# Kernel optimization log

Measured on AMD Instinct MI355X. Metric: run time of the kernel, lower is better.

Reference implementation:

```python
import jax, jax.numpy as jnp
import numpy as np

V, B, T, H = 32000, 32, 128, 256  # vocab, batch, max seq len, RNN_HIDDEN_SIZE


def setup_inputs() -> dict:
    key = jax.random.key(0)
    ks = jax.random.split(key, 16)
    stdv = 1.0 / np.sqrt(H)
    u = lambda k, shape: jax.random.uniform(k, shape, jnp.float32, -stdv, stdv)
    return {
        "tokens": jax.random.randint(ks[0], (B, T), 0, V),          # argmax of one-hot packed data
        "lengths": jax.random.randint(ks[1], (B,), 1, T + 1),        # valid lengths per sequence
        "emb": jax.random.normal(ks[2], (V, H), jnp.float32),        # tied embedding / output proj
        "Wh0": u(ks[3], (H, H)), "Wx0": u(ks[4], (H, H)), "Wy0": u(ks[5], (H, H)),
        "bh0": jnp.zeros((H,), jnp.float32), "by0": jnp.zeros((H,), jnp.float32),
        "Wh1": u(ks[6], (H, H)), "Wx1": u(ks[7], (H, H)), "Wy1": u(ks[8], (H, H)),
        "bh1": jnp.zeros((H,), jnp.float32), "by1": jnp.zeros((H,), jnp.float32),
    }


def _rnn_cell(x, Wh, Wx, bh, Wy, by):
    # x: [B, T, H]. hidden = tanh(h @ Wh + x_t @ Wx + bh); Y_t = hidden @ Wy + by
    xw = jnp.einsum('bth,hk->btk', x, Wx) + bh  # precompute input projection for all steps
    h0 = jnp.zeros((x.shape[0], Wh.shape[1]), x.dtype)

    def step(h, xt):
        h = jnp.tanh(h @ Wh + xt)
        return h, h @ Wy + by

    _, ys = jax.lax.scan(step, h0, xw.transpose(1, 0, 2))  # [T, B, H]
    return ys.transpose(1, 0, 2)  # [B, T, H]


def reference(tokens, lengths, emb, Wh0, Wx0, Wy0, bh0, by0, Wh1, Wx1, Wy1, bh1, by1):
    x = emb[tokens]                                  # embedding lookup [B, T, H]
    h = _rnn_cell(x, Wh0, Wx0, bh0, Wy0, by0)        # RNNCell layer 0
    h = _rnn_cell(h, Wh1, Wx1, bh1, Wy1, by1)        # RNNCell layer 1
    logits = jnp.einsum('bth,vh->btv', h, emb)       # hidden.data @ embedding.weight.T
    probs = jax.nn.softmax(logits, axis=-1)          # softmax over vocab
    # emulate PackedSequence: zero out padded timesteps (packed data == masked positions)
    mask = (jnp.arange(T)[None, :] < lengths[:, None]).astype(probs.dtype)  # [B, T]
    return probs * mask[:, :, None], h * mask[:, :, None]
```

## Files before the change

kernel.cpp:

```cpp
#include <hip/hip_runtime.h>
#include <hip/hip_bf16.h>


typedef _Float16 f16x8 __attribute__((ext_vector_type(8)));
typedef _Float16 f16x4 __attribute__((ext_vector_type(4)));
typedef float f32x4 __attribute__((ext_vector_type(4)));

#define NROWS 4096
#define HDIM 256
#define VOC 32000
#define VT 128
#define NVT 250

__device__ __forceinline__ float tanh_fast(float x) {
    float e = __expf(2.f * x);
    return 1.f - 2.f / (e + 1.f);
}

__global__ __launch_bounds__(256) void cvt_kernel(const float* __restrict__ in,
                                                  _Float16* __restrict__ out, int n4) {
    int i = blockIdx.x * 256 + threadIdx.x;
    if (i < n4) {
        float4 v = ((const float4*)in)[i];
        f16x4 o = {(_Float16)v.x, (_Float16)v.y, (_Float16)v.z, (_Float16)v.w};
        ((f16x4*)out)[i] = o;
    }
}

__global__ __launch_bounds__(256) void wc_kernel(const float* __restrict__ Wy0,
                                                 const float* __restrict__ Wx1,
                                                 const float* __restrict__ by0,
                                                 const float* __restrict__ bh1,
                                                 float* __restrict__ Wc,
                                                 float* __restrict__ bc) {
    __shared__ float arow[HDIM];
    int i = blockIdx.x, n = threadIdx.x;
    const float* src = (i < HDIM) ? (Wy0 + i * HDIM) : by0;
    arow[n] = src[n];
    __syncthreads();
    float acc = 0.f;
#pragma unroll 8
    for (int j = 0; j < HDIM; ++j) acc += arow[j] * Wx1[j * HDIM + n];
    if (i < HDIM) Wc[i * HDIM + n] = acc;
    else bc[n] = acc + bh1[n];
}

__global__ __launch_bounds__(256) void gemm_rows(const float* __restrict__ A,
                                                 const int* __restrict__ tokens,
                                                 const float* __restrict__ emb,
                                                 const float* __restrict__ W,
                                                 const float* __restrict__ bias,
                                                 float* __restrict__ outp,
                                                 _Float16* __restrict__ y16,
                                                 const int* __restrict__ lengths) {
    __shared__ float As[16][HDIM];
    int tid = threadIdx.x;
    int r0 = blockIdx.x * 16;
#pragma unroll
    for (int i = 0; i < 16; ++i) {
        int row = r0 + i;
        float v;
        if (tokens) v = emb[(size_t)tokens[row] * HDIM + tid];
        else        v = A[(size_t)row * HDIM + tid];
        As[i][tid] = v;
    }
    __syncthreads();
    int n = tid;
    float acc[16];
#pragma unroll
    for (int r = 0; r < 16; ++r) acc[r] = 0.f;
#pragma unroll 4
    for (int j = 0; j < HDIM; ++j) {
        float wv = W[j * HDIM + n];
#pragma unroll
        for (int r = 0; r < 16; ++r) acc[r] += As[r][j] * wv;
    }
    float bb = bias[n];
#pragma unroll
    for (int r = 0; r < 16; ++r) {
        int row = r0 + r;
        float val = acc[r] + bb;
        if (y16) {
            y16[(size_t)row * HDIM + n] = (_Float16)val;
            int b = row >> 7, t = row & 127;
            outp[(size_t)row * HDIM + n] = (t < lengths[b]) ? val : 0.f;
        } else {
            outp[(size_t)row * HDIM + n] = val;
        }
    }
}

__global__ __launch_bounds__(1024, 4) void scan_kernel(const float* __restrict__ xw,
                                                       const float* __restrict__ Wh,
                                                       float* __restrict__ hseq) {
    int b = blockIdx.x;
    int tid = threadIdx.x;
    int k = tid & 255, q = tid >> 8;
    float w[64];
#pragma unroll
    for (int j = 0; j < 64; ++j) w[j] = Wh[(q * 64 + j) * HDIM + k];
    __shared__ float hbuf[2][HDIM];
    __shared__ float psum[4][HDIM];
    if (tid < HDIM) hbuf[0][tid] = 0.f;
    __syncthreads();
    const float* xwb = xw + (size_t)b * 128 * HDIM;
    float* hb = hseq + (size_t)b * 128 * HDIM;
    for (int t = 0; t < 128; ++t) {
        int cur = t & 1;
        float xwv = 0.f;
        if (tid < HDIM) xwv = xwb[t * HDIM + tid];
        const float4* h4 = (const float4*)(&hbuf[cur][q * 64]);
        float acc = 0.f;
#pragma unroll
        for (int jj = 0; jj < 16; ++jj) {
            float4 hv = h4[jj];
            acc += w[jj * 4 + 0] * hv.x + w[jj * 4 + 1] * hv.y +
                   w[jj * 4 + 2] * hv.z + w[jj * 4 + 3] * hv.w;
        }
        psum[q][k] = acc;
        __syncthreads();
        if (tid < HDIM) {
            float s = psum[0][tid] + psum[1][tid] + psum[2][tid] + psum[3][tid] + xwv;
            float hn = tanh_fast(s);
            hbuf[1 - cur][tid] = hn;
            hb[t * HDIM + tid] = hn;
        }
        __syncthreads();
    }
}

__global__ __launch_bounds__(256) void logits_kernel(const _Float16* __restrict__ y16,
                                                     const _Float16* __restrict__ emb16,
                                                     const int* __restrict__ lengths,
                                                     float* __restrict__ probs,
                                                     float* __restrict__ partials) {
    int rt = blockIdx.x, vt = blockIdx.y;
    int r0 = rt * 16, v0 = vt * VT;
    int b = r0 >> 7, t0 = r0 & 127;
    int len = lengths[b];
    int tid = threadIdx.x, lane = tid & 63, wv = tid >> 6;

    if (len <= t0) {
        float4 z = {0.f, 0.f, 0.f, 0.f};
#pragma unroll
        for (int i = 0; i < 2; ++i) {
            int fid = tid + i * 256;
            int rl = fid >> 5, c4 = fid & 31;
            ((float4*)(probs + (size_t)(r0 + rl) * VOC + v0))[c4] = z;
        }
        return;
    }

    f32x4 acc0 = {0.f, 0.f, 0.f, 0.f}, acc1 = {0.f, 0.f, 0.f, 0.f};
    int l15 = lane & 15, quad = lane >> 4;
    int kq = quad * 8;
    const f16x8* Ap = (const f16x8*)(y16 + (size_t)(r0 + l15) * HDIM + kq);
    int n0 = v0 + wv * 32;
    const f16x8* B0 = (const f16x8*)(emb16 + (size_t)(n0 + l15) * HDIM + kq);
    const f16x8* B1 = (const f16x8*)(emb16 + (size_t)(n0 + 16 + l15) * HDIM + kq);
#pragma unroll
    for (int kk = 0; kk < 8; ++kk) {
        f16x8 af = Ap[kk * 4];
        f16x8 b0 = B0[kk * 4];
        f16x8 b1 = B1[kk * 4];
        acc0 = __builtin_amdgcn_mfma_f32_16x16x32_f16(af, b0, acc0, 0, 0, 0);
        acc1 = __builtin_amdgcn_mfma_f32_16x16x32_f16(af, b1, acc1, 0, 0, 0);
    }

    __shared__ float wsum[4][16];
    float rs[4];
#pragma unroll
    for (int r = 0; r < 4; ++r) {
        int rl = quad * 4 + r;
        bool ok = (t0 + rl) < len;
        float e0 = ok ? __expf(acc0[r]) : 0.f;
        float e1 = ok ? __expf(acc1[r]) : 0.f;
        size_t base = (size_t)(r0 + rl) * VOC;
        probs[base + n0 + l15] = e0;
        probs[base + n0 + 16 + l15] = e1;
        rs[r] = e0 + e1;
    }
#pragma unroll
    for (int m = 1; m < 16; m <<= 1) {
#pragma unroll
        for (int r = 0; r < 4; ++r) rs[r] += __shfl_xor(rs[r], m, 64);
    }
    if (l15 == 0) {
#pragma unroll
        for (int r = 0; r < 4; ++r) wsum[wv][quad * 4 + r] = rs[r];
    }
    __syncthreads();
    if (tid < 16) {
        float s = wsum[0][tid] + wsum[1][tid] + wsum[2][tid] + wsum[3][tid];
        partials[(size_t)(r0 + tid) * 256 + vt] = s;
    }
}

__global__ __launch_bounds__(256) void rescale_kernel(float* __restrict__ probs,
                                                      const float* __restrict__ partials,
                                                      const int* __restrict__ lengths) {
    int row = blockIdx.x;
    int b = row >> 7, t = row & 127;
    if (t >= lengths[b]) return;
    int tid = threadIdx.x;
    float v = (tid < NVT) ? partials[(size_t)row * 256 + tid] : 0.f;
#pragma unroll
    for (int m = 32; m >= 1; m >>= 1) v += __shfl_xor(v, m, 64);
    __shared__ float wsh[4];
    __shared__ float tot;
    if ((tid & 63) == 0) wsh[tid >> 6] = v;
    __syncthreads();
    if (tid == 0) tot = 1.f / (wsh[0] + wsh[1] + wsh[2] + wsh[3]);
    __syncthreads();
    float inv = tot;
    float* rowp = probs + (size_t)row * VOC;
#pragma unroll 5
    for (int i = 0; i < 125; ++i) rowp[i * 256 + tid] *= inv;
}

extern "C" void kernel_launch(void* const* d_in, const int* in_sizes, int n_in,
                              void* d_out, int out_size, void* d_ws, size_t ws_size,
                              hipStream_t stream) {
    const int*   tokens  = (const int*)d_in[0];
    const int*   lengths = (const int*)d_in[1];
    const float* emb     = (const float*)d_in[2];
    const float* Wh0     = (const float*)d_in[3];
    const float* Wx0     = (const float*)d_in[4];
    const float* Wy0     = (const float*)d_in[5];
    const float* bh0     = (const float*)d_in[6];
    const float* Wh1     = (const float*)d_in[8];
    const float* Wx1     = (const float*)d_in[9];
    const float* Wy1     = (const float*)d_in[10];
    const float* bh1     = (const float*)d_in[11];
    const float* by1     = (const float*)d_in[12];
    const float* by0     = (const float*)d_in[7];

    float* probs = (float*)d_out;
    float* hout  = probs + (size_t)NROWS * VOC;

    char* ws = (char*)d_ws;
    const size_t SZ_ROWS = (size_t)NROWS * HDIM * 4;
    float*     xw0     = (float*)(ws);
    float*     h0seq   = (float*)(ws + SZ_ROWS);
    float*     xw1     = (float*)(ws + 2 * SZ_ROWS);
    float*     h1seq   = (float*)(ws + 3 * SZ_ROWS);
    _Float16*  y16     = (_Float16*)(ws + 4 * SZ_ROWS);
    _Float16*  emb16   = (_Float16*)(ws + 4 * SZ_ROWS + (size_t)NROWS * HDIM * 2);
    char*      after   = ws + 4 * SZ_ROWS + (size_t)NROWS * HDIM * 2 + (size_t)VOC * HDIM * 2;
    float*     Wc      = (float*)after;
    float*     bcv     = Wc + HDIM * HDIM;
    float*     partials = (float*)(after + (HDIM * HDIM + HDIM) * 4 + 1024);

    cvt_kernel<<<8000, 256, 0, stream>>>(emb, emb16, (VOC * HDIM) / 4);
    wc_kernel<<<257, 256, 0, stream>>>(Wy0, Wx1, by0, bh1, Wc, bcv);
    gemm_rows<<<NROWS / 16, 256, 0, stream>>>(nullptr, tokens, emb, Wx0, bh0, xw0, nullptr, nullptr);
    scan_kernel<<<32, 1024, 0, stream>>>(xw0, Wh0, h0seq);
    gemm_rows<<<NROWS / 16, 256, 0, stream>>>(h0seq, nullptr, nullptr, Wc, bcv, xw1, nullptr, nullptr);
    scan_kernel<<<32, 1024, 0, stream>>>(xw1, Wh1, h1seq);
    gemm_rows<<<NROWS / 16, 256, 0, stream>>>(h1seq, nullptr, nullptr, Wy1, by1, hout, y16, lengths);
    logits_kernel<<<dim3(NROWS / 16, NVT), 256, 0, stream>>>(y16, emb16, lengths, probs, partials);
    rescale_kernel<<<NROWS, 256, 0, stream>>>(probs, partials, lengths);
}
```

Baseline: 1.613 ms.

## Recompute logits in two passes instead of writing and rescaling probs

Replaces the write-exp-then-rescale scheme with a two-pass softmax. The first pass only computes row sums of exp, a small kernel inverts them, and the second pass recomputes the GEMM and writes normalized probabilities once. The GEMM tiles also grow to 64x256 per block with more MFMA accumulators per wave for better operand reuse. The aim is to remove the extra read-modify-write of the large probs tensor, at the cost of doing the logits GEMM twice and using more registers.

```diff
diff --git a/kernel.cpp b/kernel.cpp
--- a/kernel.cpp
+++ b/kernel.cpp
@@ -9,8 +9,7 @@
 #define NROWS 4096
 #define HDIM 256
 #define VOC 32000
-#define VT 128
-#define NVT 250
+#define NVT2 125
 
 __device__ __forceinline__ float tanh_fast(float x) {
     float e = __expf(2.f * x);
@@ -129,93 +128,121 @@
     }
 }
 
-__global__ __launch_bounds__(256) void logits_kernel(const _Float16* __restrict__ y16,
-                                                     const _Float16* __restrict__ emb16,
-                                                     const int* __restrict__ lengths,
-                                                     float* __restrict__ probs,
-                                                     float* __restrict__ partials) {
+template <bool WRITE>
+__global__ __launch_bounds__(256) void softmax_gemm(const _Float16* __restrict__ y16,
+                                                    const _Float16* __restrict__ emb16,
+                                                    const int* __restrict__ lengths,
+                                                    float* __restrict__ probs,
+                                                    float* __restrict__ partials,
+                                                    const float* __restrict__ inv) {
     int rt = blockIdx.x, vt = blockIdx.y;
-    int r0 = rt * 16, v0 = vt * VT;
+    int r0 = rt * 64, v0 = vt * 256;
     int b = r0 >> 7, t0 = r0 & 127;
     int len = lengths[b];
-    int tid = threadIdx.x, lane = tid & 63, wv = tid >> 6;
+    int tid = threadIdx.x;
 
     if (len <= t0) {
-        float4 z = {0.f, 0.f, 0.f, 0.f};
-#pragma unroll
-        for (int i = 0; i < 2; ++i) {
-            int fid = tid + i * 256;
-            int rl = fid >> 5, c4 = fid & 31;
-            ((float4*)(probs + (size_t)(r0 + rl) * VOC + v0))[c4] = z;
+        if (WRITE) {
+            float4 z = {0.f, 0.f, 0.f, 0.f};
+#pragma unroll
+            for (int i = 0; i < 16; ++i) {
+                int fid = tid + i * 256;
+                int rl = fid >> 6, c4 = fid & 63;
+                ((float4*)(probs + (size_t)(r0 + rl) * VOC + v0))[c4] = z;
+            }
         }
         return;
     }
 
-    f32x4 acc0 = {0.f, 0.f, 0.f, 0.f}, acc1 = {0.f, 0.f, 0.f, 0.f};
+    int lane = tid & 63, w = tid >> 6;
     int l15 = lane & 15, quad = lane >> 4;
-    int kq = quad * 8;
-    const f16x8* Ap = (const f16x8*)(y16 + (size_t)(r0 + l15) * HDIM + kq);
-    int n0 = v0 + wv * 32;
-    const f16x8* B0 = (const f16x8*)(emb16 + (size_t)(n0 + l15) * HDIM + kq);
-    const f16x8* B1 = (const f16x8*)(emb16 + (size_t)(n0 + 16 + l15) * HDIM + kq);
+    int rw = r0 + (w & 1) * 32;
+    int nb = v0 + (w >> 1) * 128;
+    const f16x8* Ap = (const f16x8*)(y16 + (size_t)(rw + l15) * HDIM + quad * 8);
+    const f16x8* Bp = (const f16x8*)(emb16 + (size_t)(nb + l15) * HDIM + quad * 8);
+
+    f32x4 acc[2][8];
+#pragma unroll
+    for (int m = 0; m < 2; ++m)
+#pragma unroll
+        for (int i = 0; i < 8; ++i) acc[m][i] = (f32x4){0.f, 0.f, 0.f, 0.f};
+
 #pragma unroll
     for (int kk = 0; kk < 8; ++kk) {
-        f16x8 af = Ap[kk * 4];
-        f16x8 b0 = B0[kk * 4];
-        f16x8 b1 = B1[kk * 4];
-        acc0 = __builtin_amdgcn_mfma_f32_16x16x32_f16(af, b0, acc0, 0, 0, 0);
-        acc1 = __builtin_amdgcn_mfma_f32_16x16x32_f16(af, b1, acc1, 0, 0, 0);
-    }
-
-    __shared__ float wsum[4][16];
-    float rs[4];
-#pragma unroll
-    for (int r = 0; r < 4; ++r) {
-        int rl = quad * 4 + r;
-        bool ok = (t0 + rl) < len;
-        float e0 = ok ? __expf(acc0[r]) : 0.f;
-        float e1 = ok ? __expf(acc1[r]) : 0.f;
-        size_t base = (size_t)(r0 + rl) * VOC;
-        probs[base + n0 + l15] = e0;
-        probs[base + n0 + 16 + l15] = e1;
-        rs[r] = e0 + e1;
-    }
-#pragma unroll
-    for (int m = 1; m < 16; m <<= 1) {
-#pragma unroll
-        for (int r = 0; r < 4; ++r) rs[r] += __shfl_xor(rs[r], m, 64);
-    }
-    if (l15 == 0) {
-#pragma unroll
-        for (int r = 0; r < 4; ++r) wsum[wv][quad * 4 + r] = rs[r];
-    }
-    __syncthreads();
-    if (tid < 16) {
-        float s = wsum[0][tid] + wsum[1][tid] + wsum[2][tid] + wsum[3][tid];
-        partials[(size_t)(r0 + tid) * 256 + vt] = s;
-    }
-}
-
-__global__ __launch_bounds__(256) void rescale_kernel(float* __restrict__ probs,
-                                                      const float* __restrict__ partials,
-                                                      const int* __restrict__ lengths) {
-    int row = blockIdx.x;
-    int b = row >> 7, t = row & 127;
-    if (t >= lengths[b]) return;
-    int tid = threadIdx.x;
-    float v = (tid < NVT) ? partials[(size_t)row * 256 + tid] : 0.f;
-#pragma unroll
-    for (int m = 32; m >= 1; m >>= 1) v += __shfl_xor(v, m, 64);
-    __shared__ float wsh[4];
-    __shared__ float tot;
-    if ((tid & 63) == 0) wsh[tid >> 6] = v;
-    __syncthreads();
-    if (tid == 0) tot = 1.f / (wsh[0] + wsh[1] + wsh[2] + wsh[3]);
-    __syncthreads();
-    float inv = tot;
-    float* rowp = probs + (size_t)row * VOC;
-#pragma unroll 5
-    for (int i = 0; i < 125; ++i) rowp[i * 256 + tid] *= inv;
+        f16x8 a0 = Ap[kk * 4];
+        f16x8 a1 = Ap[512 + kk * 4];
+#pragma unroll
+        for (int i = 0; i < 8; ++i) {
+            f16x8 bf = Bp[i * 512 + kk * 4];
+            acc[0][i] = __builtin_amdgcn_mfma_f32_16x16x32_f16(a0, bf, acc[0][i], 0, 0, 0);
+            acc[1][i] = __builtin_amdgcn_mfma_f32_16x16x32_f16(a1, bf, acc[1][i], 0, 0, 0);
+        }
+    }
+
+    if (!WRITE) {
+        float rsum[2][4];
+#pragma unroll
+        for (int m = 0; m < 2; ++m)
+#pragma unroll
+            for (int r = 0; r < 4; ++r) {
+                float s = 0.f;
+#pragma unroll
+                for (int i = 0; i < 8; ++i) s += __expf(acc[m][i][r]);
+                rsum[m][r] = s;
+            }
+#pragma unroll
+        for (int d = 1; d < 16; d <<= 1)
+#pragma unroll
+            for (int m = 0; m < 2; ++m)
+#pragma unroll
+                for (int r = 0; r < 4; ++r)
+                    rsum[m][r] += __shfl_xor(rsum[m][r], d, 64);
+        __shared__ float ps[2][64];
+        if (l15 == 0) {
+#pragma unroll
+            for (int m = 0; m < 2; ++m)
+#pragma unroll
+                for (int r = 0; r < 4; ++r)
+                    ps[w >> 1][(w & 1) * 32 + m * 16 + quad * 4 + r] = rsum[m][r];
+        }
+        __syncthreads();
+        if (tid < 64)
+            partials[(size_t)(r0 + tid) * 128 + vt] = ps[0][tid] + ps[1][tid];
+    } else {
+        float invv[2][4];
+#pragma unroll
+        for (int m = 0; m < 2; ++m)
+#pragma unroll
+            for (int r = 0; r < 4; ++r)
+                invv[m][r] = inv[rw + m * 16 + quad * 4 + r];
+#pragma unroll
+        for (int m = 0; m < 2; ++m) {
+#pragma unroll
+            for (int r = 0; r < 4; ++r) {
+                int row = rw + m * 16 + quad * 4 + r;
+                bool ok = (row & 127) < len;
+                float iv = invv[m][r];
+                size_t base = (size_t)row * VOC + nb + l15;
+#pragma unroll
+                for (int i = 0; i < 8; ++i) {
+                    float val = ok ? __expf(acc[m][i][r]) * iv : 0.f;
+                    probs[base + i * 16] = val;
+                }
+            }
+        }
+    }
+}
+
+__global__ __launch_bounds__(128) void reduce_kernel(const float* __restrict__ partials,
+                                                     float* __restrict__ inv) {
+    int row = blockIdx.x, tid = threadIdx.x;
+    float v = (tid < NVT2) ? partials[(size_t)row * 128 + tid] : 0.f;
+#pragma unroll
+    for (int d = 1; d < 64; d <<= 1) v += __shfl_xor(v, d, 64);
+    __shared__ float s2[2];
+    if ((tid & 63) == 0) s2[tid >> 6] = v;
+    __syncthreads();
+    if (tid == 0) inv[row] = 1.f / (s2[0] + s2[1]);
 }
 
 extern "C" void kernel_launch(void* const* d_in, const int* in_sizes, int n_in,
@@ -228,12 +255,12 @@
     const float* Wx0     = (const float*)d_in[4];
     const float* Wy0     = (const float*)d_in[5];
     const float* bh0     = (const float*)d_in[6];
+    const float* by0     = (const float*)d_in[7];
     const float* Wh1     = (const float*)d_in[8];
     const float* Wx1     = (const float*)d_in[9];
     const float* Wy1     = (const float*)d_in[10];
     const float* bh1     = (const float*)d_in[11];
     const float* by1     = (const float*)d_in[12];
-    const float* by0     = (const float*)d_in[7];
 
     float* probs = (float*)d_out;
     float* hout  = probs + (size_t)NROWS * VOC;
@@ -250,6 +277,7 @@
     float*     Wc      = (float*)after;
     float*     bcv     = Wc + HDIM * HDIM;
     float*     partials = (float*)(after + (HDIM * HDIM + HDIM) * 4 + 1024);
+    float*     invp    = partials + (size_t)NROWS * 128;
 
     cvt_kernel<<<8000, 256, 0, stream>>>(emb, emb16, (VOC * HDIM) / 4);
     wc_kernel<<<257, 256, 0, stream>>>(Wy0, Wx1, by0, bh1, Wc, bcv);
@@ -258,6 +286,7 @@
     gemm_rows<<<NROWS / 16, 256, 0, stream>>>(h0seq, nullptr, nullptr, Wc, bcv, xw1, nullptr, nullptr);
     scan_kernel<<<32, 1024, 0, stream>>>(xw1, Wh1, h1seq);
     gemm_rows<<<NROWS / 16, 256, 0, stream>>>(h1seq, nullptr, nullptr, Wy1, by1, hout, y16, lengths);
-    logits_kernel<<<dim3(NROWS / 16, NVT), 256, 0, stream>>>(y16, emb16, lengths, probs, partials);
-    rescale_kernel<<<NROWS, 256, 0, stream>>>(probs, partials, lengths);
-}
+    softmax_gemm<false><<<dim3(64, NVT2), 256, 0, stream>>>(y16, emb16, lengths, nullptr, partials, nullptr);
+    reduce_kernel<<<NROWS, 128, 0, stream>>>(partials, invp);
+    softmax_gemm<true><<<dim3(64, NVT2), 256, 0, stream>>>(y16, emb16, lengths, probs, nullptr, invp);
+}
```

New measurement: 1.437 ms. 10.9% less time.
